# Optimization experiments

Measured on AMD Instinct MI355X. Metric: run time of the kernel, lower is better.

The kernel has to match this reference:

```python
import jax, jax.numpy as jnp
import numpy as np

NUM_RBF = 16
MAX_REL = 32          # max_relative_feature
AUTOREGRESSIVE = True
D_MIN, D_MAX = 2.0, 22.0
LN_EPS = 1e-5


def setup_inputs() -> dict:
    key = jax.random.key(0)
    ks = jax.random.split(key, 6)
    B, L, A, K = 1, 1280, 14, 30
    E_feat, edge_in = 128, 16 + NUM_RBF * 4 * 10  # 656
    X = jax.random.normal(ks[0], (B, L, A, 3), dtype=jnp.float32) * 3.0
    residue_idx = jnp.tile(jnp.arange(L, dtype=jnp.int32)[None], (B, 1))
    chain_labels = jnp.zeros((B, L), dtype=jnp.int32)
    E_idx = jax.random.randint(ks[1], (B, L, K), 0, L, dtype=jnp.int32)
    atom_mask = jnp.ones((B, L, A), dtype=jnp.float32)
    W_pos = jax.random.normal(ks[2], (2 * MAX_REL + 2, 16), dtype=jnp.float32) * 0.1
    b_pos = jnp.zeros((16,), dtype=jnp.float32)
    W_edge = jax.random.normal(ks[3], (edge_in, E_feat), dtype=jnp.float32) * 0.05
    ln_gamma = jnp.ones((E_feat,), dtype=jnp.float32)
    ln_beta = jnp.zeros((E_feat,), dtype=jnp.float32)
    return {"X": X, "residue_idx": residue_idx, "chain_labels": chain_labels,
            "E_idx": E_idx, "atom_mask": atom_mask, "W_pos": W_pos,
            "b_pos": b_pos, "W_edge": W_edge, "ln_gamma": ln_gamma,
            "ln_beta": ln_beta}


def _forward(X, residue_idx, chain_labels, E_idx, W_pos, b_pos, W_edge,
             ln_gamma, ln_beta):
    B, L, A, _ = X.shape
    K = E_idx.shape[-1]
    # backbone atoms in loop order [Ca, N, C, O] -> X indices [1, 0, 2, 3]
    bb = X[:, :, jnp.array([1, 0, 2, 3]), :]          # [B, L, 4, 3]
    sc = X[:, :, 4:, :]                               # [B, L, 10, 3]
    Abb = jnp.transpose(bb, (0, 2, 1, 3))             # [B, 4, L, 3]
    Asc = jnp.transpose(sc, (0, 2, 1, 3))             # [B, 10, L, 3]
    # dense pairwise distances for all 40 (bb, sc) atom pairs: [B,4,10,L,L]
    diff = Abb[:, :, None, :, None, :] - Asc[:, None, :, None, :, :]
    D = jnp.sqrt(jnp.sum(diff * diff, axis=-1) + 1e-6)
    # gather top-k neighbor columns -> [B,4,10,L,K]
    D_nb = jnp.take_along_axis(D, E_idx[:, None, None, :, :], axis=4)
    mu = jnp.linspace(D_MIN, D_MAX, NUM_RBF, dtype=D_nb.dtype)
    sigma = (D_MAX - D_MIN) / NUM_RBF
    RBF = jnp.exp(-(((D_nb[..., None] - mu) / sigma) ** 2))  # [B,4,10,L,K,16]
    if AUTOREGRESSIVE:
        self_edges = (E_idx == jnp.arange(L, dtype=E_idx.dtype)[None, :, None])
        RBF = jnp.where(self_edges[:, None, None, :, :, None], 0.0, RBF)
    # concat order: bb outer, sc inner -> [B,L,K, 4*10*16]
    RBF_all = jnp.transpose(RBF, (0, 3, 4, 1, 2, 5)).reshape(B, L, K, 4 * 10 * NUM_RBF)
    # positional encodings
    offset = residue_idx[:, :, None] - residue_idx[:, None, :]        # [B,L,L]
    offset = jnp.take_along_axis(offset, E_idx, axis=2)               # [B,L,K]
    d_chains = (chain_labels[:, :, None] == chain_labels[:, None, :]).astype(jnp.int32)
    E_chains = jnp.take_along_axis(d_chains, E_idx, axis=2)           # [B,L,K]
    d = jnp.clip(offset + MAX_REL, 0, 2 * MAX_REL) * E_chains + (1 - E_chains) * (2 * MAX_REL + 1)
    d_onehot = jax.nn.one_hot(d, 2 * MAX_REL + 2, dtype=W_pos.dtype)  # [B,L,K,66]
    E_positional = d_onehot @ W_pos + b_pos                           # [B,L,K,16]
    E = jnp.concatenate([E_positional, RBF_all], axis=-1)             # [B,L,K,656]
    E = E @ W_edge                                                    # no bias
    # LayerNorm over last dim
    mean = jnp.mean(E, axis=-1, keepdims=True)
    var = jnp.mean((E - mean) ** 2, axis=-1, keepdims=True)
    E = (E - mean) / jnp.sqrt(var + LN_EPS) * ln_gamma + ln_beta
    return E


def reference(X, residue_idx, chain_labels, E_idx, atom_mask, W_pos, b_pos,
              W_edge, ln_gamma, ln_beta):
    E = _forward(X, residue_idx, chain_labels, E_idx, W_pos, b_pos, W_edge,
                 ln_gamma, ln_beta)
    return (E, E_idx)
```

## Files before the change

kernel.cpp:

```cpp
#include <hip/hip_runtime.h>

typedef short bf16x8 __attribute__((ext_vector_type(8)));
typedef float f32x4  __attribute__((ext_vector_type(4)));

#define L_RES 1280
#define A_ATM 14
#define K_NB  30
#define FEAT  656
#define KPAD  672
#define NCH   128
#define AF_STRIDE 680
#define E_OUT_OFF (L_RES * K_NB * NCH)

__device__ __forceinline__ ushort f2bf(float x) {
    union { float f; unsigned u; } v; v.f = x;
    unsigned r = (v.u + 0x7fffu + ((v.u >> 16) & 1u)) >> 16;
    return (ushort)r;
}

__global__ __launch_bounds__(256) void wt_convert_kernel(const float* __restrict__ W,
                                                         ushort* __restrict__ Wt) {
    int idx = blockIdx.x * 256 + threadIdx.x;
    if (idx >= NCH * KPAD) return;
    int n = idx / KPAD, k = idx - n * KPAD;
    float v = (k < FEAT) ? W[k * NCH + n] : 0.0f;
    Wt[idx] = f2bf(v);
}

__global__ __launch_bounds__(256, 3) void sidechain_feat_kernel(
    const float* __restrict__ X,
    const int*   __restrict__ ridx,
    const int*   __restrict__ clab,
    const int*   __restrict__ Eidx,
    const float* __restrict__ Wpos,
    const float* __restrict__ bpos,
    const ushort* __restrict__ Wt,
    const float* __restrict__ gamma,
    const float* __restrict__ beta,
    float* __restrict__ out)
{
    __shared__ __align__(16) ushort Af[32][AF_STRIDE];
    __shared__ float bbs[4][3];
    __shared__ int   nbr[K_NB];
    __shared__ __align__(16) float part[32][4][2];

    const int i = blockIdx.x;
    const int t = threadIdx.x;
    const int w = t >> 6;
    const int lane = t & 63;
    const int frow = lane & 15;
    const int quad = lane >> 4;
    const int c0 = (2 * w) * 16 + frow;
    const int c1 = c0 + 16;

    const ushort* B0p = Wt + (size_t)c0 * KPAD + quad * 8;
    const ushort* B1p = Wt + (size_t)c1 * KPAD + quad * 8;
    bf16x8 b0c = *(const bf16x8*)(B0p);
    bf16x8 b1c = *(const bf16x8*)(B1p);
    bf16x8 b0n = *(const bf16x8*)(B0p + 32);
    bf16x8 b1n = *(const bf16x8*)(B1p + 32);
    float gg0 = gamma[c0], gg1 = gamma[c1];
    float be0 = beta[c0],  be1 = beta[c1];

    if (t < 12) {
        const int perm[4] = {1, 0, 2, 3};
        int a = t / 3, c = t - a * 3;
        bbs[a][c] = X[(i * A_ATM + perm[a]) * 3 + c];
    }
    if (t < K_NB) nbr[t] = Eidx[i * K_NB + t];
    __syncthreads();

    const int my_clab = clab[i];
    const int my_ridx = ridx[i];

#pragma unroll
    for (int u = 0; u < 2; ++u) {
        int idx = t + u * 256;
        if (idx < K_NB * 16) {
            int e = idx >> 4, c = idx & 15;
            int j = nbr[e];
            int d;
            if (my_clab == clab[j]) {
                int off = my_ridx - ridx[j] + 32;
                d = off < 0 ? 0 : (off > 64 ? 64 : off);
            } else {
                d = 65;
            }
            Af[e][c] = f2bf(Wpos[d * 16 + c] + bpos[c]);
        }
    }
#pragma unroll
    for (int u = 0; u < 2; ++u) {
        int k = t + u * 256;
        if (k < K_NB * 16) Af[k >> 4][FEAT + (k & 15)] = 0;
    }
#pragma unroll
    for (int u = 0; u < 5; ++u) {
        int idx = t + u * 256;
        if (idx < K_NB * 40) {
            int e  = idx / 40;
            int p  = idx - e * 40;
            int ab = p / 10, as = p - ab * 10;
            int j = nbr[e];
            const float* xp = X + (size_t)(j * A_ATM + 4 + as) * 3;
            float dx = bbs[ab][0] - xp[0];
            float dy = bbs[ab][1] - xp[1];
            float dz = bbs[ab][2] - xp[2];
            float dist = sqrtf(dx * dx + dy * dy + dz * dz + 1e-6f);
            bool self = (j == i);
            unsigned* dst = (unsigned*)&Af[e][16 + p * 16];
#pragma unroll
            for (int q = 0; q < 8; ++q) {
                float m0 = 2.0f + (float)(2 * q)     * (20.0f / 15.0f);
                float m1 = 2.0f + (float)(2 * q + 1) * (20.0f / 15.0f);
                float a0 = (dist - m0) * 0.8f;
                float a1 = (dist - m1) * 0.8f;
                float r0 = self ? 0.0f : __expf(-a0 * a0);
                float r1 = self ? 0.0f : __expf(-a1 * a1);
                unsigned pk;
                asm("v_cvt_pk_bf16_f32 %0, %1, %2" : "=v"(pk) : "v"(r0), "v"(r1));
                dst[q] = pk;
            }
        }
    }
    __syncthreads();

    const ushort* A0p = &Af[frow][quad * 8];
    const ushort* A1p = &Af[16 + frow][quad * 8];
    bf16x8 a0c = *(const bf16x8*)(A0p);
    bf16x8 a1c = *(const bf16x8*)(A1p);

    f32x4 acc00 = {0.f,0.f,0.f,0.f}, acc01 = {0.f,0.f,0.f,0.f};
    f32x4 acc10 = {0.f,0.f,0.f,0.f}, acc11 = {0.f,0.f,0.f,0.f};

#pragma unroll
    for (int c = 0; c < 21; ++c) {
        bf16x8 ua0 = a0c, ua1 = a1c, ub0 = b0c, ub1 = b1c;
        if (c + 1 < 21) {
            a0c = *(const bf16x8*)(A0p + (c + 1) * 32);
            a1c = *(const bf16x8*)(A1p + (c + 1) * 32);
        }
        b0c = b0n; b1c = b1n;
        if (c + 2 < 21) {
            b0n = *(const bf16x8*)(B0p + (c + 2) * 32);
            b1n = *(const bf16x8*)(B1p + (c + 2) * 32);
        }
        acc00 = __builtin_amdgcn_mfma_f32_16x16x32_bf16(ua0, ub0, acc00, 0, 0, 0);
        acc01 = __builtin_amdgcn_mfma_f32_16x16x32_bf16(ua0, ub1, acc01, 0, 0, 0);
        acc10 = __builtin_amdgcn_mfma_f32_16x16x32_bf16(ua1, ub0, acc10, 0, 0, 0);
        acc11 = __builtin_amdgcn_mfma_f32_16x16x32_bf16(ua1, ub1, acc11, 0, 0, 0);
    }

    float s0[4], q0[4], s1[4], q1[4];
#pragma unroll
    for (int r = 0; r < 4; ++r) {
        s0[r] = acc00[r] + acc01[r];
        q0[r] = acc00[r] * acc00[r] + acc01[r] * acc01[r];
        s1[r] = acc10[r] + acc11[r];
        q1[r] = acc10[r] * acc10[r] + acc11[r] * acc11[r];
    }
#pragma unroll
    for (int off = 1; off < 16; off <<= 1) {
#pragma unroll
        for (int r = 0; r < 4; ++r) {
            s0[r] += __shfl_xor(s0[r], off);
            q0[r] += __shfl_xor(q0[r], off);
            s1[r] += __shfl_xor(s1[r], off);
            q1[r] += __shfl_xor(q1[r], off);
        }
    }
    if (frow == 0) {
#pragma unroll
        for (int r = 0; r < 4; ++r) {
            int row = quad * 4 + r;
            part[row][w][0]      = s0[r];
            part[row][w][1]      = q0[r];
            part[16 + row][w][0] = s1[r];
            part[16 + row][w][1] = q1[r];
        }
    }
    __syncthreads();

#pragma unroll
    for (int r = 0; r < 4; ++r) {
        int row = quad * 4 + r;
        {
            f32x4 pa = *(const f32x4*)&part[row][0][0];
            f32x4 pb = *(const f32x4*)&part[row][2][0];
            float S = pa[0] + pa[2] + pb[0] + pb[2];
            float Q = pa[1] + pa[3] + pb[1] + pb[3];
            float mean = S * (1.0f / 128.0f);
            float rstd = rsqrtf(Q * (1.0f / 128.0f) - mean * mean + 1e-5f);
            float* o = out + (size_t)(i * K_NB + row) * NCH;
            o[c0] = (acc00[r] - mean) * rstd * gg0 + be0;
            o[c1] = (acc01[r] - mean) * rstd * gg1 + be1;
        }
        int row1 = 16 + row;
        if (row1 < K_NB) {
            f32x4 pa = *(const f32x4*)&part[row1][0][0];
            f32x4 pb = *(const f32x4*)&part[row1][2][0];
            float S = pa[0] + pa[2] + pb[0] + pb[2];
            float Q = pa[1] + pa[3] + pb[1] + pb[3];
            float mean = S * (1.0f / 128.0f);
            float rstd = rsqrtf(Q * (1.0f / 128.0f) - mean * mean + 1e-5f);
            float* o = out + (size_t)(i * K_NB + row1) * NCH;
            o[c0] = (acc10[r] - mean) * rstd * gg0 + be0;
            o[c1] = (acc11[r] - mean) * rstd * gg1 + be1;
        }
    }

    if (t < K_NB) out[E_OUT_OFF + i * K_NB + t] = (float)nbr[t];
}

extern "C" void kernel_launch(void* const* d_in, const int* in_sizes, int n_in,
                              void* d_out, int out_size, void* d_ws, size_t ws_size,
                              hipStream_t stream) {
    const float* X     = (const float*)d_in[0];
    const int*   ridx  = (const int*)  d_in[1];
    const int*   clab  = (const int*)  d_in[2];
    const int*   Eidx  = (const int*)  d_in[3];
    const float* Wpos  = (const float*)d_in[5];
    const float* bpos  = (const float*)d_in[6];
    const float* Wedge = (const float*)d_in[7];
    const float* gamma = (const float*)d_in[8];
    const float* beta  = (const float*)d_in[9];
    float* out = (float*)d_out;

    ushort* Wt = (ushort*)d_ws;

    wt_convert_kernel<<<(NCH * KPAD + 255) / 256, 256, 0, stream>>>(Wedge, Wt);
    sidechain_feat_kernel<<<L_RES, 256, 0, stream>>>(
        X, ridx, clab, Eidx, Wpos, bpos, Wt, gamma, beta, out);
}
```

Before: 103.7 us.

## Split each residue's neighbors across two blocks to halve LDS and raise occupancy

Each residue is now handled by two blocks, each covering 15 of the 30 neighbors with a single 16-row MFMA tile. This halves the LDS footprint per block and raises the launch-bounds occupancy hint from 3 to 7 blocks per CU, aiming for more concurrency and better latency hiding. The shared backbone and neighbor staging is replaced with direct global loads. The cost is that every block reloads the full weight slice, doubling weight traffic, and one of the 16 MFMA rows is padding.

```diff
diff --git a/kernel.cpp b/kernel.cpp
--- a/kernel.cpp
+++ b/kernel.cpp
@@ -6,6 +6,7 @@
 #define L_RES 1280
 #define A_ATM 14
 #define K_NB  30
+#define EPB   15
 #define FEAT  656
 #define KPAD  672
 #define NCH   128
@@ -27,7 +28,7 @@
     Wt[idx] = f2bf(v);
 }
 
-__global__ __launch_bounds__(256, 3) void sidechain_feat_kernel(
+__global__ __launch_bounds__(256, 7) void sidechain_feat_kernel(
     const float* __restrict__ X,
     const int*   __restrict__ ridx,
     const int*   __restrict__ clab,
@@ -39,18 +40,19 @@
     const float* __restrict__ beta,
     float* __restrict__ out)
 {
-    __shared__ __align__(16) ushort Af[32][AF_STRIDE];
-    __shared__ float bbs[4][3];
-    __shared__ int   nbr[K_NB];
-    __shared__ __align__(16) float part[32][4][2];
+    __shared__ __align__(16) ushort Af[16][AF_STRIDE];
+    __shared__ __align__(16) float part[16][4][2];
 
-    const int i = blockIdx.x;
-    const int t = threadIdx.x;
-    const int w = t >> 6;
+    const int blk  = blockIdx.x;
+    const int i    = blk >> 1;
+    const int h    = blk & 1;
+    const int ebase = h * EPB;
+    const int t    = threadIdx.x;
+    const int w    = t >> 6;
     const int lane = t & 63;
     const int frow = lane & 15;
     const int quad = lane >> 4;
-    const int c0 = (2 * w) * 16 + frow;
+    const int c0 = w * 32 + frow;
     const int c1 = c0 + 16;
 
     const ushort* B0p = Wt + (size_t)c0 * KPAD + quad * 8;
@@ -62,50 +64,40 @@
     float gg0 = gamma[c0], gg1 = gamma[c1];
     float be0 = beta[c0],  be1 = beta[c1];
 
-    if (t < 12) {
-        const int perm[4] = {1, 0, 2, 3};
-        int a = t / 3, c = t - a * 3;
-        bbs[a][c] = X[(i * A_ATM + perm[a]) * 3 + c];
-    }
-    if (t < K_NB) nbr[t] = Eidx[i * K_NB + t];
-    __syncthreads();
+    if (t < EPB)
+        out[E_OUT_OFF + i * K_NB + ebase + t] = (float)Eidx[i * K_NB + ebase + t];
 
     const int my_clab = clab[i];
     const int my_ridx = ridx[i];
 
+    if (t < EPB * 16) {
+        int e = t >> 4, c = t & 15;
+        int j = Eidx[i * K_NB + ebase + e];
+        int d;
+        if (my_clab == clab[j]) {
+            int off = my_ridx - ridx[j] + 32;
+            d = off < 0 ? 0 : (off > 64 ? 64 : off);
+        } else {
+            d = 65;
+        }
+        Af[e][c] = f2bf(Wpos[d * 16 + c] + bpos[c]);
+    }
+    if (t < EPB * 16) Af[t >> 4][FEAT + (t & 15)] = 0;
+
 #pragma unroll
-    for (int u = 0; u < 2; ++u) {
+    for (int u = 0; u < 3; ++u) {
         int idx = t + u * 256;
-        if (idx < K_NB * 16) {
-            int e = idx >> 4, c = idx & 15;
-            int j = nbr[e];
-            int d;
-            if (my_clab == clab[j]) {
-                int off = my_ridx - ridx[j] + 32;
-                d = off < 0 ? 0 : (off > 64 ? 64 : off);
-            } else {
-                d = 65;
-            }
-            Af[e][c] = f2bf(Wpos[d * 16 + c] + bpos[c]);
-        }
-    }
-#pragma unroll
-    for (int u = 0; u < 2; ++u) {
-        int k = t + u * 256;
-        if (k < K_NB * 16) Af[k >> 4][FEAT + (k & 15)] = 0;
-    }
-#pragma unroll
-    for (int u = 0; u < 5; ++u) {
-        int idx = t + u * 256;
-        if (idx < K_NB * 40) {
+        if (idx < EPB * 40) {
             int e  = idx / 40;
             int p  = idx - e * 40;
             int ab = p / 10, as = p - ab * 10;
-            int j = nbr[e];
+            const int perm[4] = {1, 0, 2, 3};
+            int j = Eidx[i * K_NB + ebase + e];
+            const float* xb = X + (size_t)(i * A_ATM + perm[ab]) * 3;
             const float* xp = X + (size_t)(j * A_ATM + 4 + as) * 3;
-            float dx = bbs[ab][0] - xp[0];
-            float dy = bbs[ab][1] - xp[1];
-            float dz = bbs[ab][2] - xp[2];
+            float dx = xb[0] - xp[0];
+            float dy = xb[1] - xp[1];
+            float dz = xb[2] - xp[2];
             float dist = sqrtf(dx * dx + dy * dy + dz * dz + 1e-6f);
             bool self = (j == i);
             unsigned* dst = (unsigned*)&Af[e][16 + p * 16];
@@ -126,20 +118,15 @@
     __syncthreads();
 
     const ushort* A0p = &Af[frow][quad * 8];
-    const ushort* A1p = &Af[16 + frow][quad * 8];
     bf16x8 a0c = *(const bf16x8*)(A0p);
-    bf16x8 a1c = *(const bf16x8*)(A1p);
 
     f32x4 acc00 = {0.f,0.f,0.f,0.f}, acc01 = {0.f,0.f,0.f,0.f};
-    f32x4 acc10 = {0.f,0.f,0.f,0.f}, acc11 = {0.f,0.f,0.f,0.f};
 
 #pragma unroll
     for (int c = 0; c < 21; ++c) {
-        bf16x8 ua0 = a0c, ua1 = a1c, ub0 = b0c, ub1 = b1c;
-        if (c + 1 < 21) {
+        bf16x8 ua0 = a0c, ub0 = b0c, ub1 = b1c;
+        if (c + 1 < 21)
             a0c = *(const bf16x8*)(A0p + (c + 1) * 32);
-            a1c = *(const bf16x8*)(A1p + (c + 1) * 32);
-        }
         b0c = b0n; b1c = b1n;
         if (c + 2 < 21) {
             b0n = *(const bf16x8*)(B0p + (c + 2) * 32);
@@ -147,17 +134,13 @@
         }
         acc00 = __builtin_amdgcn_mfma_f32_16x16x32_bf16(ua0, ub0, acc00, 0, 0, 0);
         acc01 = __builtin_amdgcn_mfma_f32_16x16x32_bf16(ua0, ub1, acc01, 0, 0, 0);
-        acc10 = __builtin_amdgcn_mfma_f32_16x16x32_bf16(ua1, ub0, acc10, 0, 0, 0);
-        acc11 = __builtin_amdgcn_mfma_f32_16x16x32_bf16(ua1, ub1, acc11, 0, 0, 0);
     }
 
-    float s0[4], q0[4], s1[4], q1[4];
+    float s0[4], q0[4];
 #pragma unroll
     for (int r = 0; r < 4; ++r) {
         s0[r] = acc00[r] + acc01[r];
         q0[r] = acc00[r] * acc00[r] + acc01[r] * acc01[r];
-        s1[r] = acc10[r] + acc11[r];
-        q1[r] = acc10[r] * acc10[r] + acc11[r] * acc11[r];
     }
 #pragma unroll
     for (int off = 1; off < 16; off <<= 1) {
@@ -165,18 +148,14 @@
         for (int r = 0; r < 4; ++r) {
             s0[r] += __shfl_xor(s0[r], off);
             q0[r] += __shfl_xor(q0[r], off);
-            s1[r] += __shfl_xor(s1[r], off);
-            q1[r] += __shfl_xor(q1[r], off);
         }
     }
     if (frow == 0) {
 #pragma unroll
         for (int r = 0; r < 4; ++r) {
             int row = quad * 4 + r;
-            part[row][w][0]      = s0[r];
-            part[row][w][1]      = q0[r];
-            part[16 + row][w][0] = s1[r];
-            part[16 + row][w][1] = q1[r];
+            part[row][w][0] = s0[r];
+            part[row][w][1] = q0[r];
         }
     }
     __syncthreads();
@@ -184,32 +163,18 @@
 #pragma unroll
     for (int r = 0; r < 4; ++r) {
         int row = quad * 4 + r;
-        {
+        if (row < EPB) {
             f32x4 pa = *(const f32x4*)&part[row][0][0];
             f32x4 pb = *(const f32x4*)&part[row][2][0];
             float S = pa[0] + pa[2] + pb[0] + pb[2];
             float Q = pa[1] + pa[3] + pb[1] + pb[3];
             float mean = S * (1.0f / 128.0f);
             float rstd = rsqrtf(Q * (1.0f / 128.0f) - mean * mean + 1e-5f);
-            float* o = out + (size_t)(i * K_NB + row) * NCH;
+            float* o = out + (size_t)(i * K_NB + ebase + row) * NCH;
             o[c0] = (acc00[r] - mean) * rstd * gg0 + be0;
             o[c1] = (acc01[r] - mean) * rstd * gg1 + be1;
         }
-        int row1 = 16 + row;
-        if (row1 < K_NB) {
-            f32x4 pa = *(const f32x4*)&part[row1][0][0];
-            f32x4 pb = *(const f32x4*)&part[row1][2][0];
-            float S = pa[0] + pa[2] + pb[0] + pb[2];
-            float Q = pa[1] + pa[3] + pb[1] + pb[3];
-            float mean = S * (1.0f / 128.0f);
-            float rstd = rsqrtf(Q * (1.0f / 128.0f) - mean * mean + 1e-5f);
-            float* o = out + (size_t)(i * K_NB + row1) * NCH;
-            o[c0] = (acc10[r] - mean) * rstd * gg0 + be0;
-            o[c1] = (acc11[r] - mean) * rstd * gg1 + be1;
-        }
     }
-
-    if (t < K_NB) out[E_OUT_OFF + i * K_NB + t] = (float)nbr[t];
 }
 
 extern "C" void kernel_launch(void* const* d_in, const int* in_sizes, int n_in,
@@ -229,6 +194,6 @@
     ushort* Wt = (ushort*)d_ws;
 
     wt_convert_kernel<<<(NCH * KPAD + 255) / 256, 256, 0, stream>>>(Wedge, Wt);
-    sidechain_feat_kernel<<<L_RES, 256, 0, stream>>>(
+    sidechain_feat_kernel<<<2 * L_RES, 256, 0, stream>>>(
         X, ridx, clab, Eidx, Wpos, bpos, Wt, gamma, beta, out);
 }
```

Measured after the change: 109.9 us. 1.06x slower.
